# Kernel tuning notes

Hardware: AMD Instinct MI355X
Metric: run time of the kernel (lower is better)

The kernel has to match this reference:

```python
import jax, jax.numpy as jnp
import numpy as np

NUM_HEADS = 16
NUM_KV_HEADS = 4
HEAD_DIM = 128
HALF_DIM = HEAD_DIM // 2
LAMBDA_INIT = 0.8
LAMBDA_MIN = 0.0
LAMBDA_MAX = 1.0
CAUSAL = True
NORMALIZE_DIFF = True
NEG = -1.0e9


def setup_inputs() -> dict:
    key = jax.random.key(0)
    k1, k2, k3 = jax.random.split(key, 3)
    B, Sq, Sk = 1, 2048, 2048
    query = jax.random.normal(k1, (B, NUM_HEADS, Sq, HEAD_DIM), dtype=jnp.float32)
    key_t = jax.random.normal(k2, (B, NUM_KV_HEADS, Sk, HEAD_DIM), dtype=jnp.float32)
    value = jax.random.normal(k3, (B, NUM_KV_HEADS, Sk, HEAD_DIM), dtype=jnp.float32)
    return {"query": query, "key": key_t, "value": value}


def reference(query, key, value):
    scale = 1.0 / (HALF_DIM ** 0.5)
    lam = jnp.clip(jnp.float32(LAMBDA_INIT), LAMBDA_MIN, LAMBDA_MAX)
    # GQA: repeat KV heads to match query heads
    rep = NUM_HEADS // NUM_KV_HEADS
    k = jnp.repeat(key, rep, axis=1)    # [b,h,k,d]
    v = jnp.repeat(value, rep, axis=1)  # [b,h,k,d]
    q1, q2 = query[..., :HALF_DIM], query[..., HALF_DIM:]
    k1, k2 = k[..., :HALF_DIM], k[..., HALF_DIM:]
    scores1 = jnp.einsum('bhqd,bhkd->bhqk', q1, k1) * scale
    scores2 = jnp.einsum('bhqd,bhkd->bhqk', q2, k2) * scale
    if CAUSAL:
        Sq, Sk = query.shape[2], k.shape[2]
        mask = jnp.tril(jnp.ones((Sq, Sk), dtype=jnp.float32))  # lower-triangular causal
        scores1 = scores1 * mask + (1.0 - mask) * NEG
        scores2 = scores2 * mask + (1.0 - mask) * NEG
    attn1 = jax.nn.softmax(scores1, axis=-1)
    attn2 = jax.nn.softmax(scores2, axis=-1)
    diff_attn = attn1 - lam * attn2
    out = jnp.einsum('bhqk,bhkd->bhqd', diff_attn, v)
    if NORMALIZE_DIFF:
        out = out * (1.0 - LAMBDA_INIT)
    return out
```

## Files before the change

kernel.cpp:

```cpp
#include <hip/hip_runtime.h>

#define NUM_HEADS 16
#define HEAD_DIM  128
#define SEQ       2048
#define KT_STRIDE 8192

typedef __attribute__((ext_vector_type(8))) unsigned short us8;
typedef __attribute__((ext_vector_type(8))) __bf16 bf16x8;
typedef __attribute__((ext_vector_type(4))) float f32x4;
typedef __attribute__((ext_vector_type(16))) float f32x16;
typedef __attribute__((ext_vector_type(4))) unsigned u32x4;

static __device__ inline unsigned short f2bf(float x) {
    union { float f; unsigned u; } v; v.f = x;
    unsigned r = v.u + 0x7FFFu + ((v.u >> 16) & 1u);
    return (unsigned short)(r >> 16);
}
static __device__ inline float bf2f(unsigned short h) {
    union { float f; unsigned u; } v; v.u = ((unsigned)h) << 16;
    return v.f;
}
static __device__ inline unsigned pk2bf(float a, float b) {
    return (unsigned)f2bf(a) | ((unsigned)f2bf(b) << 16);
}
static __device__ inline float fast_exp2(float x) {
#if __has_builtin(__builtin_amdgcn_exp2f)
    return __builtin_amdgcn_exp2f(x);
#else
    return exp2f(x);
#endif
}
static __device__ inline f32x16 mfma32(us8 a, us8 b, f32x16 c) {
    return __builtin_amdgcn_mfma_f32_32x32x16_bf16(
        __builtin_bit_cast(bf16x8, a), __builtin_bit_cast(bf16x8, b), c, 0, 0, 0);
}

__global__ __launch_bounds__(256)
void prep_frag(const float* __restrict__ K, const float* __restrict__ V,
               unsigned short* __restrict__ KF, unsigned short* __restrict__ VF)
{
    const int bx  = (int)blockIdx.x, t = (int)threadIdx.x;
    const int which = bx & 1, kt = (bx >> 1) & 31, kvh = bx >> 6;
    __shared__ __align__(16) float Ls[64][132];

    const float* src = (which ? V : K) + ((size_t)kvh * SEQ + kt * 64) * HEAD_DIM;
    #pragma unroll
    for (int i = 0; i < 8; ++i) {
        const int idx = t + i * 256;
        const int r = idx >> 5, c4 = idx & 31;
        *(float4*)&Ls[r][c4 * 4] = *(const float4*)(src + (size_t)r * HEAD_DIM + c4 * 4);
    }
    __syncthreads();

    if (!which) {
        #pragma unroll
        for (int i = 0; i < 4; ++i) {
            const int c = t + i * 256;
            const int lane = c & 63, ds = (c >> 6) & 3, mat = (c >> 8) & 1, kh = c >> 9;
            const int H = lane >> 5;
            const int row = kh * 32 + (lane & 31);
            const int dim = mat * 64 + ds * 16 + H * 8;
            u32x4 pk;
            #pragma unroll
            for (int jj = 0; jj < 4; ++jj)
                pk[jj] = pk2bf(Ls[row][dim + 2*jj], Ls[row][dim + 2*jj + 1]);
            *(us8*)(KF + ((size_t)(kvh * 32 + kt) * 16 + kh * 8 + mat * 4 + ds) * 512 + lane * 8)
                = __builtin_bit_cast(us8, pk);
        }
    } else {
        #pragma unroll
        for (int i = 0; i < 4; ++i) {
            const int c = t + i * 256;
            const int lane = c & 63, db = (c >> 6) & 3, ks = (c >> 8) & 1, kh = c >> 9;
            const int H = lane >> 5;
            const int s0 = kh * 32 + ks * 16 + H * 8;
            const int d  = db * 32 + (lane & 31);
            u32x4 pk;
            #pragma unroll
            for (int jj = 0; jj < 4; ++jj)
                pk[jj] = pk2bf(Ls[s0 + 2*jj][d], Ls[s0 + 2*jj + 1][d]);
            *(us8*)(VF + ((size_t)(kvh * 32 + kt) * 16 + kh * 8 + ks * 4 + db) * 512 + lane * 8)
                = __builtin_bit_cast(us8, pk);
        }
    }
}

__global__ __launch_bounds__(256, 2)
void diff_attn_mfma7(const float* __restrict__ Q,
                     const unsigned short* __restrict__ KF,
                     const unsigned short* __restrict__ VF,
                     float* __restrict__ Out)
{
    __shared__ float cb[2][32][136];
    __shared__ float rsb[2][2][32];

    const int t   = (int)threadIdx.x;
    const int wv  = t >> 6;
    const int ln  = t & 63;
    const int mat = wv >> 1;
    const int kh  = wv & 1;
    const int q   = ln & 31;
    const int H   = ln >> 5;

    const int bx   = (int)blockIdx.x;
    const int h    = bx & 15;
    const int idx  = bx >> 4;
    const int qtA  = idx, qtB = 63 - idx;
    const int nktA = (qtA >> 1) + 1;
    const int kvh  = h >> 2;

    const unsigned short* kfb = KF + ((size_t)kvh * 32 * 16 + kh * 8 + mat * 4) * 512 + ln * 8;
    const unsigned short* vfb = VF + ((size_t)kvh * 32 * 16 + kh * 8) * 512 + ln * 8;

    const float qscale = 0.125f * 1.44269504088896340736f;

    us8 qhi[4], qlo[4];
    auto loadQ = [&](int q0c) {
        const float* qr = Q + ((size_t)h * SEQ + q0c + q) * HEAD_DIM + mat * 64;
        #pragma unroll
        for (int ds = 0; ds < 4; ++ds) {
            const int d0 = ds * 16 + H * 8;
            float x[8];
            *(float4*)&x[0] = *(const float4*)(qr + d0);
            *(float4*)&x[4] = *(const float4*)(qr + d0 + 4);
            us8 hi8, lo8;
            #pragma unroll
            for (int j = 0; j < 8; ++j) {
                float xs = x[j] * qscale;
                unsigned short hb = f2bf(xs);
                hi8[j] = hb;
                lo8[j] = f2bf(xs - bf2f(hb));
            }
            qhi[ds] = hi8; qlo[ds] = lo8;
        }
    };

    f32x16 o[4];
    f32x4  rsv = (f32x4)0.f;
    #pragma unroll
    for (int i = 0; i < 4; ++i) o[i] = (f32x16)0.f;

    auto epilogue = [&](int q0c) {
        __syncthreads();
        float rsc = (rsv[0] + rsv[1]) + (rsv[2] + rsv[3]);
        rsc += __shfl_xor(rsc, 32, 64);
        if (ln < 32) rsb[mat][kh][ln] = rsc;
        if (kh == 1) {
            #pragma unroll
            for (int db = 0; db < 4; ++db)
                #pragma unroll
                for (int i = 0; i < 4; ++i) {
                    float4 v = { o[db][i*4+0], o[db][i*4+1], o[db][i*4+2], o[db][i*4+3] };
                    *(float4*)&cb[mat][q][db * 32 + 8 * i + 4 * H] = v;
                }
        }
        __syncthreads();
        if (kh == 0) {
            const float l = rsb[mat][0][q] + rsb[mat][1][q];
            const float a = mat ? (0.16f / l) : (0.2f / l);
            #pragma unroll
            for (int db = 0; db < 4; ++db)
                #pragma unroll
                for (int i = 0; i < 4; ++i) {
                    float4 v = *(float4*)&cb[mat][q][db * 32 + 8 * i + 4 * H];
                    o[db][i*4+0] = (o[db][i*4+0] + v.x) * a;
                    o[db][i*4+1] = (o[db][i*4+1] + v.y) * a;
                    o[db][i*4+2] = (o[db][i*4+2] + v.z) * a;
                    o[db][i*4+3] = (o[db][i*4+3] + v.w) * a;
                }
            if (mat == 1) {
                #pragma unroll
                for (int db = 0; db < 4; ++db)
                    #pragma unroll
                    for (int i = 0; i < 4; ++i) {
                        float4 v = { o[db][i*4+0], o[db][i*4+1], o[db][i*4+2], o[db][i*4+3] };
                        *(float4*)&cb[1][q][db * 32 + 8 * i + 4 * H] = v;
                    }
            }
        }
        __syncthreads();
        if (wv == 0) {
            float* ob = Out + ((size_t)h * SEQ + q0c + q) * HEAD_DIM;
            #pragma unroll
            for (int db = 0; db < 4; ++db)
                #pragma unroll
                for (int i = 0; i < 4; ++i) {
                    float4 v = *(float4*)&cb[1][q][db * 32 + 8 * i + 4 * H];
                    float4 r;
                    r.x = o[db][i*4+0] - v.x;
                    r.y = o[db][i*4+1] - v.y;
                    r.z = o[db][i*4+2] - v.z;
                    r.w = o[db][i*4+3] - v.w;
                    *(float4*)(ob + db * 32 + 8 * i + 4 * H) = r;
                }
        }
    };

    int q0 = qtA * 32, qpar = qtA & 1;
    loadQ(q0);

    us8 ka[4], kan[4], va[8];
    #pragma unroll
    for (int ds = 0; ds < 4; ++ds) ka[ds] = *(const us8*)(kfb + ds * 512);

    for (int j = 0; j < 33; ++j) {
        if (j == nktA) {
            epilogue(q0);
            q0 = qtB * 32; qpar = qtB & 1;
            loadQ(q0);
            #pragma unroll
            for (int i = 0; i < 4; ++i) o[i] = (f32x16)0.f;
            rsv = (f32x4)0.f;
        }
        const int kt = (j < nktA) ? j : j - nktA;

        {
            const unsigned short* vb = vfb + (size_t)kt * KT_STRIDE;
            #pragma unroll
            for (int c = 0; c < 8; ++c) va[c] = *(const us8*)(vb + c * 512);
        }
        if (j + 1 < 33) {
            const int nk = (j + 1 >= nktA) ? (j + 1 - nktA) : (j + 1);
            const unsigned short* kb = kfb + (size_t)nk * KT_STRIDE;
            #pragma unroll
            for (int ds = 0; ds < 4; ++ds) kan[ds] = *(const us8*)(kb + ds * 512);
        }

        const bool diag  = (j == nktA - 1) || (j == 32);
        const bool skipw = diag && (qpar == 0) && (kh == 1);
        const bool triw  = diag && (kh == qpar);

        if (!skipw) {
            f32x16 s = (f32x16)0.f;
            #pragma unroll
            for (int ds = 0; ds < 4; ++ds) {
                s = mfma32(ka[ds], qhi[ds], s);
                s = mfma32(ka[ds], qlo[ds], s);
            }
            unsigned c[16];
            if (triw) {
                const int kg0 = kt * 64 + kh * 32 + 4 * H;
                const int qg  = q0 + q;
                #pragma unroll
                for (int r = 0; r < 16; ++r) {
                    const int kg = kg0 + (r & 3) + ((r >> 2) << 3);
                    float e = (kg <= qg) ? fast_exp2(s[r]) : 0.f;
                    c[r] = __builtin_bit_cast(unsigned, e) & 0xffff0000u;
                    rsv[r & 3] += __builtin_bit_cast(float, c[r]);
                }
            } else {
                #pragma unroll
                for (int r = 0; r < 16; ++r) {
                    float e = fast_exp2(s[r]);
                    c[r] = __builtin_bit_cast(unsigned, e) & 0xffff0000u;
                    rsv[r & 3] += __builtin_bit_cast(float, c[r]);
                }
            }
            #pragma unroll
            for (int ks = 0; ks < 2; ++ks) {
                const unsigned pA = (c[8*ks+0] >> 16) | c[8*ks+1];
                const unsigned pB = (c[8*ks+2] >> 16) | c[8*ks+3];
                const unsigned pC = (c[8*ks+4] >> 16) | c[8*ks+5];
                const unsigned pD = (c[8*ks+6] >> 16) | c[8*ks+7];
                const unsigned x1 = H ? pA : pC;
                const unsigned x2 = H ? pB : pD;
                const unsigned t1 = (unsigned)__shfl_xor((int)x1, 32, 64);
                const unsigned t2 = (unsigned)__shfl_xor((int)x2, 32, 64);
                u32x4 bw;
                bw[0] = H ? t1 : pA;
                bw[1] = H ? t2 : pB;
                bw[2] = H ? pC : t1;
                bw[3] = H ? pD : t2;
                const us8 bp = __builtin_bit_cast(us8, bw);
                #pragma unroll
                for (int db = 0; db < 4; ++db)
                    o[db] = mfma32(va[ks * 4 + db], bp, o[db]);
            }
        }

        #pragma unroll
        for (int ds = 0; ds < 4; ++ds) ka[ds] = kan[ds];
    }

    epilogue(q0);
}

extern "C" void kernel_launch(void* const* d_in, const int* in_sizes, int n_in,
                              void* d_out, int out_size, void* d_ws, size_t ws_size,
                              hipStream_t stream) {
    const float* Q = (const float*)d_in[0];
    const float* K = (const float*)d_in[1];
    const float* V = (const float*)d_in[2];
    float* Out = (float*)d_out;

    unsigned short* KF = (unsigned short*)d_ws;
    unsigned short* VF = KF + (size_t)4 * SEQ * HEAD_DIM;

    prep_frag<<<256, 256, 0, stream>>>(K, V, KF, VF);
    diff_attn_mfma7<<<512, 256, 0, stream>>>(Q, KF, VF, Out);
}
```

Baseline: 116.8 us.

## Split paired causal query tiles into separate blocks, heaviest first, raise occupancy

Before, each block handled two query tiles (idx and 63-idx) so every block did the same amount of causal work. Now each block handles one 32-row query tile, and blocks are ordered so the longest tiles launch first. The grid doubles to 1024 and launch bounds ask for 3 blocks per SM, aiming for better occupancy and latency hiding. The cost is that load balance now depends on the hardware scheduler, there are more per-block prologues, and the tighter register budget could cause spilling.

```diff
diff --git a/kernel.cpp b/kernel.cpp
--- a/kernel.cpp
+++ b/kernel.cpp
@@ -85,8 +85,8 @@
     }
 }
 
-__global__ __launch_bounds__(256, 2)
-void diff_attn_mfma7(const float* __restrict__ Q,
+__global__ __launch_bounds__(256, 3)
+void diff_attn_mfma8(const float* __restrict__ Q,
                      const unsigned short* __restrict__ KF,
                      const unsigned short* __restrict__ VF,
                      float* __restrict__ Out)
@@ -104,9 +104,10 @@
 
     const int bx   = (int)blockIdx.x;
     const int h    = bx & 15;
-    const int idx  = bx >> 4;
-    const int qtA  = idx, qtB = 63 - idx;
-    const int nktA = (qtA >> 1) + 1;
+    const int qt   = 63 - (bx >> 4);
+    const int qpar = qt & 1;
+    const int nkt  = (qt >> 1) + 1;
+    const int q0   = qt * 32;
     const int kvh  = h >> 2;
 
     const unsigned short* kfb = KF + ((size_t)kvh * 32 * 16 + kh * 8 + mat * 4) * 512 + ln * 8;
@@ -115,8 +116,8 @@
     const float qscale = 0.125f * 1.44269504088896340736f;
 
     us8 qhi[4], qlo[4];
-    auto loadQ = [&](int q0c) {
-        const float* qr = Q + ((size_t)h * SEQ + q0c + q) * HEAD_DIM + mat * 64;
+    {
+        const float* qr = Q + ((size_t)h * SEQ + q0 + q) * HEAD_DIM + mat * 64;
         #pragma unroll
         for (int ds = 0; ds < 4; ++ds) {
             const int d0 = ds * 16 + H * 8;
@@ -133,100 +134,30 @@
             }
             qhi[ds] = hi8; qlo[ds] = lo8;
         }
-    };
+    }
 
     f32x16 o[4];
     f32x4  rsv = (f32x4)0.f;
     #pragma unroll
     for (int i = 0; i < 4; ++i) o[i] = (f32x16)0.f;
 
-    auto epilogue = [&](int q0c) {
-        __syncthreads();
-        float rsc = (rsv[0] + rsv[1]) + (rsv[2] + rsv[3]);
-        rsc += __shfl_xor(rsc, 32, 64);
-        if (ln < 32) rsb[mat][kh][ln] = rsc;
-        if (kh == 1) {
-            #pragma unroll
-            for (int db = 0; db < 4; ++db)
-                #pragma unroll
-                for (int i = 0; i < 4; ++i) {
-                    float4 v = { o[db][i*4+0], o[db][i*4+1], o[db][i*4+2], o[db][i*4+3] };
-                    *(float4*)&cb[mat][q][db * 32 + 8 * i + 4 * H] = v;
-                }
-        }
-        __syncthreads();
-        if (kh == 0) {
-            const float l = rsb[mat][0][q] + rsb[mat][1][q];
-            const float a = mat ? (0.16f / l) : (0.2f / l);
-            #pragma unroll
-            for (int db = 0; db < 4; ++db)
-                #pragma unroll
-                for (int i = 0; i < 4; ++i) {
-                    float4 v = *(float4*)&cb[mat][q][db * 32 + 8 * i + 4 * H];
-                    o[db][i*4+0] = (o[db][i*4+0] + v.x) * a;
-                    o[db][i*4+1] = (o[db][i*4+1] + v.y) * a;
-                    o[db][i*4+2] = (o[db][i*4+2] + v.z) * a;
-                    o[db][i*4+3] = (o[db][i*4+3] + v.w) * a;
-                }
-            if (mat == 1) {
-                #pragma unroll
-                for (int db = 0; db < 4; ++db)
-                    #pragma unroll
-                    for (int i = 0; i < 4; ++i) {
-                        float4 v = { o[db][i*4+0], o[db][i*4+1], o[db][i*4+2], o[db][i*4+3] };
-                        *(float4*)&cb[1][q][db * 32 + 8 * i + 4 * H] = v;
-                    }
-            }
-        }
-        __syncthreads();
-        if (wv == 0) {
-            float* ob = Out + ((size_t)h * SEQ + q0c + q) * HEAD_DIM;
-            #pragma unroll
-            for (int db = 0; db < 4; ++db)
-                #pragma unroll
-                for (int i = 0; i < 4; ++i) {
-                    float4 v = *(float4*)&cb[1][q][db * 32 + 8 * i + 4 * H];
-                    float4 r;
-                    r.x = o[db][i*4+0] - v.x;
-                    r.y = o[db][i*4+1] - v.y;
-                    r.z = o[db][i*4+2] - v.z;
-                    r.w = o[db][i*4+3] - v.w;
-                    *(float4*)(ob + db * 32 + 8 * i + 4 * H) = r;
-                }
-        }
-    };
-
-    int q0 = qtA * 32, qpar = qtA & 1;
-    loadQ(q0);
-
     us8 ka[4], kan[4], va[8];
     #pragma unroll
     for (int ds = 0; ds < 4; ++ds) ka[ds] = *(const us8*)(kfb + ds * 512);
 
-    for (int j = 0; j < 33; ++j) {
-        if (j == nktA) {
-            epilogue(q0);
-            q0 = qtB * 32; qpar = qtB & 1;
-            loadQ(q0);
-            #pragma unroll
-            for (int i = 0; i < 4; ++i) o[i] = (f32x16)0.f;
-            rsv = (f32x4)0.f;
-        }
-        const int kt = (j < nktA) ? j : j - nktA;
-
+    for (int j = 0; j < nkt; ++j) {
         {
-            const unsigned short* vb = vfb + (size_t)kt * KT_STRIDE;
+            const unsigned short* vb = vfb + (size_t)j * KT_STRIDE;
             #pragma unroll
             for (int c = 0; c < 8; ++c) va[c] = *(const us8*)(vb + c * 512);
         }
-        if (j + 1 < 33) {
-            const int nk = (j + 1 >= nktA) ? (j + 1 - nktA) : (j + 1);
-            const unsigned short* kb = kfb + (size_t)nk * KT_STRIDE;
+        if (j + 1 < nkt) {
+            const unsigned short* kb = kfb + (size_t)(j + 1) * KT_STRIDE;
             #pragma unroll
             for (int ds = 0; ds < 4; ++ds) kan[ds] = *(const us8*)(kb + ds * 512);
         }
 
-        const bool diag  = (j == nktA - 1) || (j == 32);
+        const bool diag  = (j == nkt - 1);
         const bool skipw = diag && (qpar == 0) && (kh == 1);
         const bool triw  = diag && (kh == qpar);
 
@@ -239,7 +170,7 @@
             }
             unsigned c[16];
             if (triw) {
-                const int kg0 = kt * 64 + kh * 32 + 4 * H;
+                const int kg0 = j * 64 + kh * 32 + 4 * H;
                 const int qg  = q0 + q;
                 #pragma unroll
                 for (int r = 0; r < 16; ++r) {
@@ -282,7 +213,59 @@
         for (int ds = 0; ds < 4; ++ds) ka[ds] = kan[ds];
     }
 
-    epilogue(q0);
+    __syncthreads();
+    float rsc = (rsv[0] + rsv[1]) + (rsv[2] + rsv[3]);
+    rsc += __shfl_xor(rsc, 32, 64);
+    if (ln < 32) rsb[mat][kh][ln] = rsc;
+    if (kh == 1) {
+        #pragma unroll
+        for (int db = 0; db < 4; ++db)
+            #pragma unroll
+            for (int i = 0; i < 4; ++i) {
+                float4 v = { o[db][i*4+0], o[db][i*4+1], o[db][i*4+2], o[db][i*4+3] };
+                *(float4*)&cb[mat][q][db * 32 + 8 * i + 4 * H] = v;
+            }
+    }
+    __syncthreads();
+    if (kh == 0) {
+        const float l = rsb[mat][0][q] + rsb[mat][1][q];
+        const float a = mat ? (0.16f / l) : (0.2f / l);
+        #pragma unroll
+        for (int db = 0; db < 4; ++db)
+            #pragma unroll
+            for (int i = 0; i < 4; ++i) {
+                float4 v = *(float4*)&cb[mat][q][db * 32 + 8 * i + 4 * H];
+                o[db][i*4+0] = (o[db][i*4+0] + v.x) * a;
+                o[db][i*4+1] = (o[db][i*4+1] + v.y) * a;
+                o[db][i*4+2] = (o[db][i*4+2] + v.z) * a;
+                o[db][i*4+3] = (o[db][i*4+3] + v.w) * a;
+            }
+        if (mat == 1) {
+            #pragma unroll
+            for (int db = 0; db < 4; ++db)
+                #pragma unroll
+                for (int i = 0; i < 4; ++i) {
+                    float4 v = { o[db][i*4+0], o[db][i*4+1], o[db][i*4+2], o[db][i*4+3] };
+                    *(float4*)&cb[1][q][db * 32 + 8 * i + 4 * H] = v;
+                }
+        }
+    }
+    __syncthreads();
+    if (wv == 0) {
+        float* ob = Out + ((size_t)h * SEQ + q0 + q) * HEAD_DIM;
+        #pragma unroll
+        for (int db = 0; db < 4; ++db)
+            #pragma unroll
+            for (int i = 0; i < 4; ++i) {
+                float4 v = *(float4*)&cb[1][q][db * 32 + 8 * i + 4 * H];
+                float4 r;
+                r.x = o[db][i*4+0] - v.x;
+                r.y = o[db][i*4+1] - v.y;
+                r.z = o[db][i*4+2] - v.z;
+                r.w = o[db][i*4+3] - v.w;
+                *(float4*)(ob + db * 32 + 8 * i + 4 * H) = r;
+            }
+    }
 }
 
 extern "C" void kernel_launch(void* const* d_in, const int* in_sizes, int n_in,
@@ -297,5 +280,5 @@
     unsigned short* VF = KF + (size_t)4 * SEQ * HEAD_DIM;
 
     prep_frag<<<256, 256, 0, stream>>>(K, V, KF, VF);
-    diff_attn_mfma7<<<512, 256, 0, stream>>>(Q, KF, VF, Out);
-}
+    diff_attn_mfma8<<<1024, 256, 0, stream>>>(Q, KF, VF, Out);
+}
```

New measurement: 162.6 us. +39.3%, slower.

## Software-pipeline QK scores one tile ahead and split loop into per-query-tile segments

Applied to the files above, without the earlier changes.

Restructures the main loop into a run_seg lambda per query tile, which computes the QK^T scores for the next key tile while the current tile's exp/pack and PV MFMAs run. K fragments are prefetched two tiles ahead. Splitting into two segments removes the per-iteration tile-switch and index branches. The cost is an extra live 16-float score accumulator, which raises register pressure under the two-blocks-per-SM launch bound. The fully masked diagonal-tile warp is no longer skipped, so it now does work that is then masked to zero.

```diff
diff --git a/kernel.cpp b/kernel.cpp
--- a/kernel.cpp
+++ b/kernel.cpp
@@ -86,7 +86,7 @@
 }
 
 __global__ __launch_bounds__(256, 2)
-void diff_attn_mfma7(const float* __restrict__ Q,
+void diff_attn_mfma9(const float* __restrict__ Q,
                      const unsigned short* __restrict__ KF,
                      const unsigned short* __restrict__ VF,
                      float* __restrict__ Out)
@@ -136,9 +136,7 @@
     };
 
     f32x16 o[4];
-    f32x4  rsv = (f32x4)0.f;
-    #pragma unroll
-    for (int i = 0; i < 4; ++i) o[i] = (f32x16)0.f;
+    f32x4  rsv;
 
     auto epilogue = [&](int q0c) {
         __syncthreads();
@@ -196,51 +194,46 @@
         }
     };
 
-    int q0 = qtA * 32, qpar = qtA & 1;
-    loadQ(q0);
-
-    us8 ka[4], kan[4], va[8];
-    #pragma unroll
-    for (int ds = 0; ds < 4; ++ds) ka[ds] = *(const us8*)(kfb + ds * 512);
-
-    for (int j = 0; j < 33; ++j) {
-        if (j == nktA) {
-            epilogue(q0);
-            q0 = qtB * 32; qpar = qtB & 1;
-            loadQ(q0);
-            #pragma unroll
-            for (int i = 0; i < 4; ++i) o[i] = (f32x16)0.f;
-            rsv = (f32x4)0.f;
-        }
-        const int kt = (j < nktA) ? j : j - nktA;
-
-        {
-            const unsigned short* vb = vfb + (size_t)kt * KT_STRIDE;
-            #pragma unroll
-            for (int c = 0; c < 8; ++c) va[c] = *(const us8*)(vb + c * 512);
-        }
-        if (j + 1 < 33) {
-            const int nk = (j + 1 >= nktA) ? (j + 1 - nktA) : (j + 1);
-            const unsigned short* kb = kfb + (size_t)nk * KT_STRIDE;
-            #pragma unroll
-            for (int ds = 0; ds < 4; ++ds) kan[ds] = *(const us8*)(kb + ds * 512);
-        }
-
-        const bool diag  = (j == nktA - 1) || (j == 32);
-        const bool skipw = diag && (qpar == 0) && (kh == 1);
-        const bool triw  = diag && (kh == qpar);
-
-        if (!skipw) {
-            f32x16 s = (f32x16)0.f;
-            #pragma unroll
-            for (int ds = 0; ds < 4; ++ds) {
-                s = mfma32(ka[ds], qhi[ds], s);
-                s = mfma32(ka[ds], qlo[ds], s);
-            }
+    auto run_seg = [&](int q0c, int nseg) {
+        us8 ka[4], kan[4], va[8];
+        #pragma unroll
+        for (int ds = 0; ds < 4; ++ds) ka[ds] = *(const us8*)(kfb + ds * 512);
+        f32x16 s = (f32x16)0.f;
+        #pragma unroll
+        for (int ds = 0; ds < 4; ++ds) {
+            s = mfma32(ka[ds], qhi[ds], s);
+            s = mfma32(ka[ds], qlo[ds], s);
+        }
+        if (nseg > 1) {
+            #pragma unroll
+            for (int ds = 0; ds < 4; ++ds) ka[ds] = *(const us8*)(kfb + KT_STRIDE + ds * 512);
+        }
+
+        for (int j = 0; j < nseg; ++j) {
+            {
+                const unsigned short* vb = vfb + (size_t)j * KT_STRIDE;
+                #pragma unroll
+                for (int c = 0; c < 8; ++c) va[c] = *(const us8*)(vb + c * 512);
+            }
+            if (j + 2 < nseg) {
+                const unsigned short* kb = kfb + (size_t)(j + 2) * KT_STRIDE;
+                #pragma unroll
+                for (int ds = 0; ds < 4; ++ds) kan[ds] = *(const us8*)(kb + ds * 512);
+            }
+
+            f32x16 sn = (f32x16)0.f;
+            if (j + 1 < nseg) {
+                #pragma unroll
+                for (int ds = 0; ds < 4; ++ds) {
+                    sn = mfma32(ka[ds], qhi[ds], sn);
+                    sn = mfma32(ka[ds], qlo[ds], sn);
+                }
+            }
+
             unsigned c[16];
-            if (triw) {
-                const int kg0 = kt * 64 + kh * 32 + 4 * H;
-                const int qg  = q0 + q;
+            if (j == nseg - 1) {
+                const int kg0 = j * 64 + kh * 32 + 4 * H;
+                const int qg  = q0c + q;
                 #pragma unroll
                 for (int r = 0; r < 16; ++r) {
                     const int kg = kg0 + (r & 3) + ((r >> 2) << 3);
@@ -256,6 +249,7 @@
                     rsv[r & 3] += __builtin_bit_cast(float, c[r]);
                 }
             }
+
             #pragma unroll
             for (int ks = 0; ks < 2; ++ks) {
                 const unsigned pA = (c[8*ks+0] >> 16) | c[8*ks+1];
@@ -276,13 +270,26 @@
                 for (int db = 0; db < 4; ++db)
                     o[db] = mfma32(va[ks * 4 + db], bp, o[db]);
             }
-        }
-
-        #pragma unroll
-        for (int ds = 0; ds < 4; ++ds) ka[ds] = kan[ds];
-    }
-
-    epilogue(q0);
+
+            #pragma unroll
+            for (int ds = 0; ds < 4; ++ds) ka[ds] = kan[ds];
+            s = sn;
+        }
+    };
+
+    loadQ(qtA * 32);
+    #pragma unroll
+    for (int i = 0; i < 4; ++i) o[i] = (f32x16)0.f;
+    rsv = (f32x4)0.f;
+    run_seg(qtA * 32, nktA);
+    epilogue(qtA * 32);
+
+    loadQ(qtB * 32);
+    #pragma unroll
+    for (int i = 0; i < 4; ++i) o[i] = (f32x16)0.f;
+    rsv = (f32x4)0.f;
+    run_seg(qtB * 32, 33 - nktA);
+    epilogue(qtB * 32);
 }
 
 extern "C" void kernel_launch(void* const* d_in, const int* in_sizes, int n_in,
@@ -297,5 +304,5 @@
     unsigned short* VF = KF + (size_t)4 * SEQ * HEAD_DIM;
 
     prep_frag<<<256, 256, 0, stream>>>(K, V, KF, VF);
-    diff_attn_mfma7<<<512, 256, 0, stream>>>(Q, KF, VF, Out);
-}
+    diff_attn_mfma9<<<512, 256, 0, stream>>>(Q, KF, VF, Out);
+}
```

Result: no change. 118.2 us (+1.3%).
